# Kernel optimization log

Measured on AMD Instinct MI355X. Metric: run time of the kernel, lower is better.

Reference implementation:

```python
import jax, jax.numpy as jnp
import numpy as np

MODEL_DIMS = 1024
NUM_LAYERS = 4
NUM_SUPPORT = 256


def setup_inputs() -> dict:
    key = jax.random.key(0)
    kx, kk, kv = jax.random.split(key, 3)
    x = jax.random.normal(kx, (4, 4096, MODEL_DIMS), dtype=jnp.float32)
    # Stacked per-layer parameters, matching nn.Parameter(torch.randn(...))
    keys = jax.random.normal(kk, (NUM_LAYERS, NUM_SUPPORT, MODEL_DIMS), dtype=jnp.float32)
    values = jax.random.normal(kv, (NUM_LAYERS, NUM_SUPPORT, MODEL_DIMS), dtype=jnp.float32)
    return {"x": x, "keys": keys, "values": values}


def reference(x, keys, values):
    # Chain of CleanUpKV layers: normalize -> scores -> softmax -> weighted values.
    def step(h, kv):
        k, v = kv  # k, v: [num_support, D]
        hn = h / (jnp.linalg.norm(h, axis=-1, keepdims=True) + 1e-9)
        scores = jnp.einsum('bsd,nd->bsn', hn, k)          # [B,S,num_support]
        w = jax.nn.softmax(scores, axis=-1)
        return jnp.einsum('bsn,nd->bsd', w, v), None

    out, _ = jax.lax.scan(step, x, (keys, values))
    return out
```

## Files before the change

### kernel.cpp

```cpp
#include <hip/hip_runtime.h>
#include <hip/hip_bf16.h>
#include <stdint.h>

#define D 1024
#define NSUP 256
#define ROWS 16384
#define MB 64
#define LTHREADS 512

typedef __attribute__((__ext_vector_type__(8))) __bf16 bf16x8;
typedef __attribute__((__ext_vector_type__(4))) float f32x4;

__device__ __forceinline__ float bfbits2f(uint32_t b) {
    union { uint32_t u; float f; } c; c.u = b; return c.f;
}

__device__ __forceinline__ int hnb(int row, int d) {
    return ((row << 8) + (d << 1)) ^ ((row & 7) << 4);
}
__device__ __forceinline__ int wbyte(int row, int n) {
    return ((row << 9) + (n << 1)) ^ ((row & 7) << 4);
}

__global__ void cast_k_kernel(const float* __restrict__ K, __bf16* __restrict__ Kb) {
    int i = (blockIdx.x * 256 + threadIdx.x) * 4;
    float4 v = *(const float4*)(K + i);
    __bf16 o[4] __attribute__((aligned(8)));
    o[0] = (__bf16)v.x; o[1] = (__bf16)v.y; o[2] = (__bf16)v.z; o[3] = (__bf16)v.w;
    *(uint2*)(Kb + i) = *(const uint2*)o;
}

__global__ void transpose_v_kernel(const float* __restrict__ V, __bf16* __restrict__ Vt) {
    __shared__ __bf16 tile[64][72];
    int l = blockIdx.z;
    int d0 = blockIdx.x * 64, n0 = blockIdx.y * 64;
    const float* Vl = V + (size_t)l * NSUP * D;
    __bf16* Vtl = Vt + (size_t)l * D * NSUP;
    for (int j = 0; j < 16; ++j) {
        int idx = j * 256 + threadIdx.x;
        int n_l = idx >> 6, d_l = idx & 63;
        tile[d_l][n_l] = (__bf16)Vl[(size_t)(n0 + n_l) * D + d0 + d_l];
    }
    __syncthreads();
    for (int j = 0; j < 16; ++j) {
        int idx = j * 256 + threadIdx.x;
        int d_l = idx >> 6, n_l = idx & 63;
        Vtl[(size_t)(d0 + d_l) * NSUP + n0 + n_l] = tile[d_l][n_l];
    }
}

__global__ void norms0_kernel(const float* __restrict__ x, float* __restrict__ rn) {
    int row = blockIdx.x * 4 + (threadIdx.x >> 6);
    int lane = threadIdx.x & 63;
    const float4* p = (const float4*)(x + (size_t)row * D);
    float s = 0.f;
    #pragma unroll
    for (int j = 0; j < 4; ++j) {
        float4 v = p[j * 64 + lane];
        s += v.x * v.x + v.y * v.y + v.z * v.z + v.w * v.w;
    }
    #pragma unroll
    for (int off = 1; off < 64; off <<= 1) s += __shfl_xor(s, off);
    if (lane == 0) rn[row] = 1.f / (sqrtf(s) + 1e-9f);
}

template<bool IN_F32, bool OUT_F32>
__global__ __launch_bounds__(LTHREADS)
void layer_kernel(const void* h_in, void* h_out,
                  const __bf16* __restrict__ Kb, const __bf16* __restrict__ Vt,
                  const float* __restrict__ rn_in, float* __restrict__ rn_out) {
    const int tid = threadIdx.x;
    const int lane = tid & 63;
    const int cg = tid >> 6;
    const int llo = lane & 15, lhi = lane >> 4;
    const int row0 = blockIdx.x * MB;

    __shared__ __align__(16) char lds_hn[2][MB * 128 * 2];
    __shared__ __align__(16) char lds_w[MB * NSUP * 2];
    __shared__ float red1[MB][8];
    __shared__ float red2[MB][8];
    __shared__ float rnin_s[MB];

    if (tid < MB) rnin_s[tid] = rn_in[row0 + tid];

    const int srow = tid >> 3;
    const int sd = (tid & 7) * 16;

    float stg[16];
    auto load_chunk = [&](int dc) {
        if constexpr (IN_F32) {
            const float4* p = (const float4*)((const float*)h_in + (size_t)(row0 + srow) * D + dc * 128 + sd);
            #pragma unroll
            for (int j = 0; j < 4; ++j) {
                float4 v = p[j];
                stg[4 * j] = v.x; stg[4 * j + 1] = v.y; stg[4 * j + 2] = v.z; stg[4 * j + 3] = v.w;
            }
        } else {
            const uint4* p = (const uint4*)((const uint16_t*)h_in + (size_t)(row0 + srow) * D + dc * 128 + sd);
            #pragma unroll
            for (int j = 0; j < 2; ++j) {
                uint4 u = p[j];
                uint32_t wv[4] = {u.x, u.y, u.z, u.w};
                #pragma unroll
                for (int q = 0; q < 4; ++q) {
                    stg[8 * j + 2 * q]     = bfbits2f(wv[q] << 16);
                    stg[8 * j + 2 * q + 1] = bfbits2f(wv[q] & 0xffff0000u);
                }
            }
        }
    };
    auto write_chunk = [&](int dc) {
        float rn = rnin_s[srow];
        __bf16 tmp[16] __attribute__((aligned(16)));
        #pragma unroll
        for (int j = 0; j < 16; ++j) tmp[j] = (__bf16)(stg[j] * rn);
        char* base = lds_hn[dc & 1];
        *(bf16x8*)(base + hnb(srow, sd))     = *(const bf16x8*)(tmp);
        *(bf16x8*)(base + hnb(srow, sd + 8)) = *(const bf16x8*)(tmp + 8);
    };

    f32x4 acc[4][2];
    #pragma unroll
    for (int rf = 0; rf < 4; ++rf)
        #pragma unroll
        for (int cf = 0; cf < 2; ++cf)
            acc[rf][cf] = (f32x4){0.f, 0.f, 0.f, 0.f};

    load_chunk(0);
    #pragma unroll 1
    for (int dc = 0; dc < 8; ++dc) {
        __syncthreads();
        write_chunk(dc);
        if (dc < 7) load_chunk(dc + 1);
        __syncthreads();
        const char* hb = lds_hn[dc & 1];
        #pragma unroll
        for (int k = 0; k < 4; ++k) {
            bf16x8 a[4];
            #pragma unroll
            for (int rf = 0; rf < 4; ++rf)
                a[rf] = *(const bf16x8*)(hb + hnb(rf * 16 + llo, k * 32 + lhi * 8));
            #pragma unroll
            for (int cf = 0; cf < 2; ++cf) {
                const __bf16* kp = Kb + (size_t)(cg * 32 + cf * 16 + llo) * D + dc * 128 + k * 32 + lhi * 8;
                bf16x8 b = *(const bf16x8*)kp;
                #pragma unroll
                for (int rf = 0; rf < 4; ++rf)
                    acc[rf][cf] = __builtin_amdgcn_mfma_f32_16x16x32_bf16(a[rf], b, acc[rf][cf], 0, 0, 0);
            }
        }
    }

    float rmax[4][4];
    #pragma unroll
    for (int rf = 0; rf < 4; ++rf)
        #pragma unroll
        for (int r = 0; r < 4; ++r) {
            float m = fmaxf(acc[rf][0][r], acc[rf][1][r]);
            #pragma unroll
            for (int off = 1; off < 16; off <<= 1) m = fmaxf(m, __shfl_xor(m, off));
            rmax[rf][r] = m;
        }
    if (llo == 0) {
        #pragma unroll
        for (int rf = 0; rf < 4; ++rf)
            #pragma unroll
            for (int r = 0; r < 4; ++r)
                red1[rf * 16 + lhi * 4 + r][cg] = rmax[rf][r];
    }
    __syncthreads();
    #pragma unroll
    for (int rf = 0; rf < 4; ++rf)
        #pragma unroll
        for (int r = 0; r < 4; ++r) {
            int row = rf * 16 + lhi * 4 + r;
            f32x4 m0 = *(const f32x4*)&red1[row][0];
            f32x4 m1 = *(const f32x4*)&red1[row][4];
            float m = fmaxf(fmaxf(fmaxf(m0[0], m0[1]), fmaxf(m0[2], m0[3])),
                            fmaxf(fmaxf(m1[0], m1[1]), fmaxf(m1[2], m1[3])));
            rmax[rf][r] = m;
        }
    float rsum[4][4];
    #pragma unroll
    for (int rf = 0; rf < 4; ++rf)
        #pragma unroll
        for (int r = 0; r < 4; ++r) {
            float s = 0.f;
            #pragma unroll
            for (int cf = 0; cf < 2; ++cf) {
                float e = exp2f((acc[rf][cf][r] - rmax[rf][r]) * 1.44269504f);
                acc[rf][cf][r] = e;
                s += e;
            }
            #pragma unroll
            for (int off = 1; off < 16; off <<= 1) s += __shfl_xor(s, off);
            rsum[rf][r] = s;
        }
    if (llo == 0) {
        #pragma unroll
        for (int rf = 0; rf < 4; ++rf)
            #pragma unroll
            for (int r = 0; r < 4; ++r)
                red2[rf * 16 + lhi * 4 + r][cg] = rsum[rf][r];
    }
    __syncthreads();
    #pragma unroll
    for (int rf = 0; rf < 4; ++rf)
        #pragma unroll
        for (int r = 0; r < 4; ++r) {
            int row = rf * 16 + lhi * 4 + r;
            f32x4 s0 = *(const f32x4*)&red2[row][0];
            f32x4 s1 = *(const f32x4*)&red2[row][4];
            float s = (s0[0] + s0[1] + s0[2] + s0[3]) + (s1[0] + s1[1] + s1[2] + s1[3]);
            float inv = 1.f / s;
            #pragma unroll
            for (int cf = 0; cf < 2; ++cf) {
                int col = cg * 32 + cf * 16 + llo;
                *(__bf16*)(lds_w + wbyte(row, col)) = (__bf16)(acc[rf][cf][r] * inv);
            }
        }
    __syncthreads();

    float nacc[4][4];
    #pragma unroll
    for (int rf = 0; rf < 4; ++rf)
        #pragma unroll
        for (int r = 0; r < 4; ++r) nacc[rf][r] = 0.f;

    #pragma unroll 1
    for (int dchunk = 0; dchunk < 2; ++dchunk) {
        f32x4 acc2[4][4];
        #pragma unroll
        for (int rf = 0; rf < 4; ++rf)
            #pragma unroll
            for (int cf = 0; cf < 4; ++cf)
                acc2[rf][cf] = (f32x4){0.f, 0.f, 0.f, 0.f};
        #pragma unroll
        for (int k = 0; k < 8; ++k) {
            bf16x8 a[4];
            #pragma unroll
            for (int rf = 0; rf < 4; ++rf)
                a[rf] = *(const bf16x8*)(lds_w + wbyte(rf * 16 + llo, k * 32 + lhi * 8));
            #pragma unroll
            for (int cf = 0; cf < 4; ++cf) {
                const __bf16* vp = Vt + (size_t)(cg * 128 + dchunk * 64 + cf * 16 + llo) * NSUP + k * 32 + lhi * 8;
                bf16x8 b = *(const bf16x8*)vp;
                #pragma unroll
                for (int rf = 0; rf < 4; ++rf)
                    acc2[rf][cf] = __builtin_amdgcn_mfma_f32_16x16x32_bf16(a[rf], b, acc2[rf][cf], 0, 0, 0);
            }
        }
        #pragma unroll
        for (int rf = 0; rf < 4; ++rf)
            #pragma unroll
            for (int cf = 0; cf < 4; ++cf) {
                int d = cg * 128 + dchunk * 64 + cf * 16 + llo;
                #pragma unroll
                for (int r = 0; r < 4; ++r) {
                    int row = rf * 16 + lhi * 4 + r;
                    float v = acc2[rf][cf][r];
                    size_t idx = (size_t)(row0 + row) * D + d;
                    if constexpr (OUT_F32) {
                        ((float*)h_out)[idx] = v;
                    } else {
                        ((__bf16*)h_out)[idx] = (__bf16)v;
                        nacc[rf][r] += v * v;
                    }
                }
            }
    }

    if constexpr (!OUT_F32) {
        #pragma unroll
        for (int rf = 0; rf < 4; ++rf)
            #pragma unroll
            for (int r = 0; r < 4; ++r) {
                float s = nacc[rf][r];
                #pragma unroll
                for (int off = 1; off < 16; off <<= 1) s += __shfl_xor(s, off);
                nacc[rf][r] = s;
            }
        if (llo == 0) {
            #pragma unroll
            for (int rf = 0; rf < 4; ++rf)
                #pragma unroll
                for (int r = 0; r < 4; ++r)
                    red1[rf * 16 + lhi * 4 + r][cg] = nacc[rf][r];
        }
        __syncthreads();
        if (cg == 0 && llo == 0) {
            #pragma unroll
            for (int rf = 0; rf < 4; ++rf)
                #pragma unroll
                for (int r = 0; r < 4; ++r) {
                    int row = rf * 16 + lhi * 4 + r;
                    f32x4 s0 = *(const f32x4*)&red1[row][0];
                    f32x4 s1 = *(const f32x4*)&red1[row][4];
                    float ss = (s0[0] + s0[1] + s0[2] + s0[3]) + (s1[0] + s1[1] + s1[2] + s1[3]);
                    rn_out[row0 + row] = 1.f / (sqrtf(ss) + 1e-9f);
                }
        }
    }
}

extern "C" void kernel_launch(void* const* d_in, const int* in_sizes, int n_in,
                              void* d_out, int out_size, void* d_ws, size_t ws_size,
                              hipStream_t stream) {
    const float* x = (const float*)d_in[0];
    const float* keys = (const float*)d_in[1];
    const float* values = (const float*)d_in[2];
    float* out = (float*)d_out;

    char* ws = (char*)d_ws;
    __bf16* h   = (__bf16*)(ws);
    __bf16* Kb  = (__bf16*)(ws + 33554432);
    __bf16* Vt  = (__bf16*)(ws + 35651584);
    float*  rn0 = (float*)(ws + 37748736);
    float*  rn1 = (float*)(ws + 37814272);

    cast_k_kernel<<<1024, 256, 0, stream>>>(keys, Kb);
    transpose_v_kernel<<<dim3(16, 4, 4), 256, 0, stream>>>(values, Vt);
    norms0_kernel<<<4096, 256, 0, stream>>>(x, rn0);

    const int LSTRIDE = NSUP * D;
    layer_kernel<true,  false><<<256, LTHREADS, 0, stream>>>(x, h, Kb,               Vt,               rn0, rn1);
    layer_kernel<false, false><<<256, LTHREADS, 0, stream>>>(h, h, Kb + LSTRIDE,     Vt + LSTRIDE,     rn1, rn0);
    layer_kernel<false, false><<<256, LTHREADS, 0, stream>>>(h, h, Kb + 2 * LSTRIDE, Vt + 2 * LSTRIDE, rn0, rn1);
    layer_kernel<false, true ><<<256, LTHREADS, 0, stream>>>(h, out, Kb + 3 * LSTRIDE, Vt + 3 * LSTRIDE, rn1, nullptr);
}
```

Before: 268.5 us.

## Halve row tile, store pre-normalized bf16 activations, use direct global-to-LDS loads

Shrinks the row block from 64 to 32, which doubles the grid to 512 blocks. Occupancy is raised with launch bounds of 4 blocks per SM. The separate norms kernel is folded into the first layer. Later layers now store normalized bf16 activations, so the next layer can stream them straight into LDS with global_load_lds and skip the per-element conversion. Output writes for intermediate layers are staged through swizzled LDS so they become coalesced 16-byte stores. In exchange, each block gets fewer MFMAs per K/V load, and global K/V traffic per row doubles.

```diff
diff --git a/kernel.cpp b/kernel.cpp
--- a/kernel.cpp
+++ b/kernel.cpp
@@ -5,22 +5,17 @@
 #define D 1024
 #define NSUP 256
 #define ROWS 16384
-#define MB 64
+#define MB 32
 #define LTHREADS 512
+#define LGRID (ROWS / MB)
 
 typedef __attribute__((__ext_vector_type__(8))) __bf16 bf16x8;
 typedef __attribute__((__ext_vector_type__(4))) float f32x4;
-
-__device__ __forceinline__ float bfbits2f(uint32_t b) {
-    union { uint32_t u; float f; } c; c.u = b; return c.f;
-}
-
-__device__ __forceinline__ int hnb(int row, int d) {
-    return ((row << 8) + (d << 1)) ^ ((row & 7) << 4);
-}
-__device__ __forceinline__ int wbyte(int row, int n) {
-    return ((row << 9) + (n << 1)) ^ ((row & 7) << 4);
-}
+typedef __attribute__((__ext_vector_type__(4))) uint32_t u32x4;
+
+#define MFMA16(a, b, c) __builtin_amdgcn_mfma_f32_16x16x32_bf16((a), (b), (c), 0, 0, 0)
+
+__device__ __forceinline__ int swz(int row, int byte) { return byte ^ ((row & 7) << 4); }
 
 __global__ void cast_k_kernel(const float* __restrict__ K, __bf16* __restrict__ Kb) {
     int i = (blockIdx.x * 256 + threadIdx.x) * 4;
@@ -49,128 +44,119 @@
     }
 }
 
-__global__ void norms0_kernel(const float* __restrict__ x, float* __restrict__ rn) {
-    int row = blockIdx.x * 4 + (threadIdx.x >> 6);
-    int lane = threadIdx.x & 63;
-    const float4* p = (const float4*)(x + (size_t)row * D);
-    float s = 0.f;
-    #pragma unroll
-    for (int j = 0; j < 4; ++j) {
-        float4 v = p[j * 64 + lane];
-        s += v.x * v.x + v.y * v.y + v.z * v.z + v.w * v.w;
-    }
-    #pragma unroll
-    for (int off = 1; off < 64; off <<= 1) s += __shfl_xor(s, off);
-    if (lane == 0) rn[row] = 1.f / (sqrtf(s) + 1e-9f);
-}
-
 template<bool IN_F32, bool OUT_F32>
-__global__ __launch_bounds__(LTHREADS)
-void layer_kernel(const void* h_in, void* h_out,
-                  const __bf16* __restrict__ Kb, const __bf16* __restrict__ Vt,
-                  const float* __restrict__ rn_in, float* __restrict__ rn_out) {
+__global__ __launch_bounds__(LTHREADS, 4)
+void layer_kernel(const void* __restrict__ h_in, void* __restrict__ h_out,
+                  const __bf16* __restrict__ Kb, const __bf16* __restrict__ Vt) {
     const int tid = threadIdx.x;
     const int lane = tid & 63;
     const int cg = tid >> 6;
     const int llo = lane & 15, lhi = lane >> 4;
     const int row0 = blockIdx.x * MB;
 
-    __shared__ __align__(16) char lds_hn[2][MB * 128 * 2];
-    __shared__ __align__(16) char lds_w[MB * NSUP * 2];
+    __shared__ __align__(16) char pool[49152];
     __shared__ float red1[MB][8];
     __shared__ float red2[MB][8];
     __shared__ float rnin_s[MB];
 
-    if (tid < MB) rnin_s[tid] = rn_in[row0 + tid];
-
-    const int srow = tid >> 3;
-    const int sd = (tid & 7) * 16;
-
-    float stg[16];
-    auto load_chunk = [&](int dc) {
+    char* wbuf = pool + 32768;
+
+    if constexpr (IN_F32) {
+        const float4* x4 = (const float4*)h_in;
+        #pragma unroll
+        for (int rr = 0; rr < 4; ++rr) {
+            int row = cg * 4 + rr;
+            const float4* p = x4 + (size_t)(row0 + row) * 256;
+            float s = 0.f;
+            #pragma unroll
+            for (int j = 0; j < 4; ++j) {
+                float4 v = p[j * 64 + lane];
+                s += v.x * v.x + v.y * v.y + v.z * v.z + v.w * v.w;
+            }
+            #pragma unroll
+            for (int off = 1; off < 64; off <<= 1) s += __shfl_xor(s, off);
+            if (lane == 0) rnin_s[row] = 1.f / (sqrtf(s) + 1e-9f);
+        }
+        __syncthreads();
+    }
+
+    auto stage = [&](int dc) {
+        char* hb = pool + (dc & 1) * 16384;
         if constexpr (IN_F32) {
-            const float4* p = (const float4*)((const float*)h_in + (size_t)(row0 + srow) * D + dc * 128 + sd);
-            #pragma unroll
-            for (int j = 0; j < 4; ++j) {
-                float4 v = p[j];
-                stg[4 * j] = v.x; stg[4 * j + 1] = v.y; stg[4 * j + 2] = v.z; stg[4 * j + 3] = v.w;
-            }
+            int srow = tid >> 4;
+            int sd = (tid & 15) * 16;
+            const float4* p = (const float4*)((const float*)h_in + (size_t)(row0 + srow) * D + dc * 256 + sd);
+            float rn = rnin_s[srow];
+            __bf16 tmp[16] __attribute__((aligned(16)));
+            #pragma unroll
+            for (int q = 0; q < 4; ++q) {
+                float4 v = p[q];
+                tmp[4 * q + 0] = (__bf16)(v.x * rn);
+                tmp[4 * q + 1] = (__bf16)(v.y * rn);
+                tmp[4 * q + 2] = (__bf16)(v.z * rn);
+                tmp[4 * q + 3] = (__bf16)(v.w * rn);
+            }
+            char* base = hb + srow * 512;
+            *(bf16x8*)(base + swz(srow, sd * 2))      = *(const bf16x8*)(tmp);
+            *(bf16x8*)(base + swz(srow, sd * 2 + 16)) = *(const bf16x8*)(tmp + 8);
         } else {
-            const uint4* p = (const uint4*)((const uint16_t*)h_in + (size_t)(row0 + srow) * D + dc * 128 + sd);
-            #pragma unroll
-            for (int j = 0; j < 2; ++j) {
-                uint4 u = p[j];
-                uint32_t wv[4] = {u.x, u.y, u.z, u.w};
-                #pragma unroll
-                for (int q = 0; q < 4; ++q) {
-                    stg[8 * j + 2 * q]     = bfbits2f(wv[q] << 16);
-                    stg[8 * j + 2 * q + 1] = bfbits2f(wv[q] & 0xffff0000u);
-                }
+            #pragma unroll
+            for (int c = 0; c < 2; ++c) {
+                int row = c * 16 + (tid >> 5);
+                int seg = tid & 31;
+                const char* g = (const char*)h_in + (size_t)(row0 + row) * 2048 + (size_t)dc * 512
+                                + swz(row, seg * 16);
+                char* l = hb + row * 512 + seg * 16;
+                __builtin_amdgcn_global_load_lds(
+                    (const __attribute__((address_space(1))) uint32_t*)g,
+                    (__attribute__((address_space(3))) uint32_t*)l, 16, 0, 0);
             }
         }
     };
-    auto write_chunk = [&](int dc) {
-        float rn = rnin_s[srow];
-        __bf16 tmp[16] __attribute__((aligned(16)));
-        #pragma unroll
-        for (int j = 0; j < 16; ++j) tmp[j] = (__bf16)(stg[j] * rn);
-        char* base = lds_hn[dc & 1];
-        *(bf16x8*)(base + hnb(srow, sd))     = *(const bf16x8*)(tmp);
-        *(bf16x8*)(base + hnb(srow, sd + 8)) = *(const bf16x8*)(tmp + 8);
-    };
-
-    f32x4 acc[4][2];
-    #pragma unroll
-    for (int rf = 0; rf < 4; ++rf)
+
+    f32x4 acc[2][2];
+    #pragma unroll
+    for (int rf = 0; rf < 2; ++rf)
         #pragma unroll
         for (int cf = 0; cf < 2; ++cf)
             acc[rf][cf] = (f32x4){0.f, 0.f, 0.f, 0.f};
 
-    load_chunk(0);
+    stage(0);
+    __syncthreads();
     #pragma unroll 1
-    for (int dc = 0; dc < 8; ++dc) {
+    for (int dc = 0; dc < 4; ++dc) {
+        if (dc < 3) stage(dc + 1);
+        const char* hb = pool + (dc & 1) * 16384;
+        #pragma unroll
+        for (int k = 0; k < 8; ++k) {
+            bf16x8 a0 = *(const bf16x8*)(hb + llo * 512 + swz(llo, k * 64 + lhi * 16));
+            bf16x8 a1 = *(const bf16x8*)(hb + (16 + llo) * 512 + swz(16 + llo, k * 64 + lhi * 16));
+            #pragma unroll
+            for (int cf = 0; cf < 2; ++cf) {
+                bf16x8 b = *(const bf16x8*)(Kb + (size_t)(cg * 32 + cf * 16 + llo) * D
+                                            + dc * 256 + k * 32 + lhi * 8);
+                acc[0][cf] = MFMA16(a0, b, acc[0][cf]);
+                acc[1][cf] = MFMA16(a1, b, acc[1][cf]);
+            }
+        }
         __syncthreads();
-        write_chunk(dc);
-        if (dc < 7) load_chunk(dc + 1);
-        __syncthreads();
-        const char* hb = lds_hn[dc & 1];
-        #pragma unroll
-        for (int k = 0; k < 4; ++k) {
-            bf16x8 a[4];
-            #pragma unroll
-            for (int rf = 0; rf < 4; ++rf)
-                a[rf] = *(const bf16x8*)(hb + hnb(rf * 16 + llo, k * 32 + lhi * 8));
-            #pragma unroll
-            for (int cf = 0; cf < 2; ++cf) {
-                const __bf16* kp = Kb + (size_t)(cg * 32 + cf * 16 + llo) * D + dc * 128 + k * 32 + lhi * 8;
-                bf16x8 b = *(const bf16x8*)kp;
-                #pragma unroll
-                for (int rf = 0; rf < 4; ++rf)
-                    acc[rf][cf] = __builtin_amdgcn_mfma_f32_16x16x32_bf16(a[rf], b, acc[rf][cf], 0, 0, 0);
-            }
-        }
-    }
-
-    float rmax[4][4];
-    #pragma unroll
-    for (int rf = 0; rf < 4; ++rf)
+    }
+
+    float rmax[2][4];
+    #pragma unroll
+    for (int rf = 0; rf < 2; ++rf)
         #pragma unroll
         for (int r = 0; r < 4; ++r) {
             float m = fmaxf(acc[rf][0][r], acc[rf][1][r]);
             #pragma unroll
             for (int off = 1; off < 16; off <<= 1) m = fmaxf(m, __shfl_xor(m, off));
             rmax[rf][r] = m;
-        }
-    if (llo == 0) {
-        #pragma unroll
-        for (int rf = 0; rf < 4; ++rf)
-            #pragma unroll
-            for (int r = 0; r < 4; ++r)
-                red1[rf * 16 + lhi * 4 + r][cg] = rmax[rf][r];
-    }
-    __syncthreads();
-    #pragma unroll
-    for (int rf = 0; rf < 4; ++rf)
+            if (llo == 0) red1[rf * 16 + lhi * 4 + r][cg] = m;
+        }
+    __syncthreads();
+    float rsum[2][4];
+    #pragma unroll
+    for (int rf = 0; rf < 2; ++rf)
         #pragma unroll
         for (int r = 0; r < 4; ++r) {
             int row = rf * 16 + lhi * 4 + r;
@@ -178,34 +164,21 @@
             f32x4 m1 = *(const f32x4*)&red1[row][4];
             float m = fmaxf(fmaxf(fmaxf(m0[0], m0[1]), fmaxf(m0[2], m0[3])),
                             fmaxf(fmaxf(m1[0], m1[1]), fmaxf(m1[2], m1[3])));
-            rmax[rf][r] = m;
-        }
-    float rsum[4][4];
-    #pragma unroll
-    for (int rf = 0; rf < 4; ++rf)
-        #pragma unroll
-        for (int r = 0; r < 4; ++r) {
             float s = 0.f;
             #pragma unroll
             for (int cf = 0; cf < 2; ++cf) {
-                float e = exp2f((acc[rf][cf][r] - rmax[rf][r]) * 1.44269504f);
+                float e = exp2f((acc[rf][cf][r] - m) * 1.44269504f);
                 acc[rf][cf][r] = e;
                 s += e;
             }
             #pragma unroll
             for (int off = 1; off < 16; off <<= 1) s += __shfl_xor(s, off);
             rsum[rf][r] = s;
-        }
-    if (llo == 0) {
-        #pragma unroll
-        for (int rf = 0; rf < 4; ++rf)
-            #pragma unroll
-            for (int r = 0; r < 4; ++r)
-                red2[rf * 16 + lhi * 4 + r][cg] = rsum[rf][r];
-    }
-    __syncthreads();
-    #pragma unroll
-    for (int rf = 0; rf < 4; ++rf)
+            if (llo == 0) red2[row][cg] = s;
+        }
+    __syncthreads();
+    #pragma unroll
+    for (int rf = 0; rf < 2; ++rf)
         #pragma unroll
         for (int r = 0; r < 4; ++r) {
             int row = rf * 16 + lhi * 4 + r;
@@ -216,89 +189,97 @@
             #pragma unroll
             for (int cf = 0; cf < 2; ++cf) {
                 int col = cg * 32 + cf * 16 + llo;
-                *(__bf16*)(lds_w + wbyte(row, col)) = (__bf16)(acc[rf][cf][r] * inv);
-            }
-        }
-    __syncthreads();
-
-    float nacc[4][4];
-    #pragma unroll
-    for (int rf = 0; rf < 4; ++rf)
-        #pragma unroll
-        for (int r = 0; r < 4; ++r) nacc[rf][r] = 0.f;
-
-    #pragma unroll 1
-    for (int dchunk = 0; dchunk < 2; ++dchunk) {
-        f32x4 acc2[4][4];
-        #pragma unroll
-        for (int rf = 0; rf < 4; ++rf)
-            #pragma unroll
-            for (int cf = 0; cf < 4; ++cf)
-                acc2[rf][cf] = (f32x4){0.f, 0.f, 0.f, 0.f};
-        #pragma unroll
-        for (int k = 0; k < 8; ++k) {
-            bf16x8 a[4];
-            #pragma unroll
-            for (int rf = 0; rf < 4; ++rf)
-                a[rf] = *(const bf16x8*)(lds_w + wbyte(rf * 16 + llo, k * 32 + lhi * 8));
-            #pragma unroll
-            for (int cf = 0; cf < 4; ++cf) {
-                const __bf16* vp = Vt + (size_t)(cg * 128 + dchunk * 64 + cf * 16 + llo) * NSUP + k * 32 + lhi * 8;
-                bf16x8 b = *(const bf16x8*)vp;
-                #pragma unroll
-                for (int rf = 0; rf < 4; ++rf)
-                    acc2[rf][cf] = __builtin_amdgcn_mfma_f32_16x16x32_bf16(a[rf], b, acc2[rf][cf], 0, 0, 0);
-            }
-        }
-        #pragma unroll
-        for (int rf = 0; rf < 4; ++rf)
-            #pragma unroll
-            for (int cf = 0; cf < 4; ++cf) {
-                int d = cg * 128 + dchunk * 64 + cf * 16 + llo;
+                *(__bf16*)(wbuf + row * 512 + swz(row, col * 2)) = (__bf16)(acc[rf][cf][r] * inv);
+            }
+        }
+    __syncthreads();
+
+    f32x4 acc2[2][8];
+    #pragma unroll
+    for (int rf = 0; rf < 2; ++rf)
+        #pragma unroll
+        for (int cf = 0; cf < 8; ++cf)
+            acc2[rf][cf] = (f32x4){0.f, 0.f, 0.f, 0.f};
+
+    #pragma unroll
+    for (int k = 0; k < 8; ++k) {
+        bf16x8 a0 = *(const bf16x8*)(wbuf + llo * 512 + swz(llo, k * 64 + lhi * 16));
+        bf16x8 a1 = *(const bf16x8*)(wbuf + (16 + llo) * 512 + swz(16 + llo, k * 64 + lhi * 16));
+        #pragma unroll
+        for (int cf = 0; cf < 8; ++cf) {
+            bf16x8 b = *(const bf16x8*)(Vt + (size_t)(cg * 128 + cf * 16 + llo) * NSUP
+                                        + k * 32 + lhi * 8);
+            acc2[0][cf] = MFMA16(a0, b, acc2[0][cf]);
+            acc2[1][cf] = MFMA16(a1, b, acc2[1][cf]);
+        }
+    }
+
+    if constexpr (OUT_F32) {
+        float* outp = (float*)h_out;
+        #pragma unroll
+        for (int rf = 0; rf < 2; ++rf)
+            #pragma unroll
+            for (int cf = 0; cf < 8; ++cf) {
+                int d = cg * 128 + cf * 16 + llo;
                 #pragma unroll
                 for (int r = 0; r < 4; ++r) {
                     int row = rf * 16 + lhi * 4 + r;
-                    float v = acc2[rf][cf][r];
-                    size_t idx = (size_t)(row0 + row) * D + d;
-                    if constexpr (OUT_F32) {
-                        ((float*)h_out)[idx] = v;
-                    } else {
-                        ((__bf16*)h_out)[idx] = (__bf16)v;
-                        nacc[rf][r] += v * v;
+                    outp[(size_t)(row0 + row) * D + d] = acc2[rf][cf][r];
+                }
+            }
+    } else {
+        float rnv[2][4];
+        #pragma unroll
+        for (int rf = 0; rf < 2; ++rf)
+            #pragma unroll
+            for (int r = 0; r < 4; ++r) {
+                float s = 0.f;
+                #pragma unroll
+                for (int cf = 0; cf < 8; ++cf) s += acc2[rf][cf][r] * acc2[rf][cf][r];
+                #pragma unroll
+                for (int off = 1; off < 16; off <<= 1) s += __shfl_xor(s, off);
+                if (llo == 0) red2[rf * 16 + lhi * 4 + r][cg] = s;
+            }
+        __syncthreads();
+        #pragma unroll
+        for (int rf = 0; rf < 2; ++rf)
+            #pragma unroll
+            for (int r = 0; r < 4; ++r) {
+                int row = rf * 16 + lhi * 4 + r;
+                f32x4 s0 = *(const f32x4*)&red2[row][0];
+                f32x4 s1 = *(const f32x4*)&red2[row][4];
+                float ss = (s0[0] + s0[1] + s0[2] + s0[3]) + (s1[0] + s1[1] + s1[2] + s1[3]);
+                rnv[rf][r] = 1.f / (sqrtf(ss) + 1e-9f);
+            }
+        const int myhalf = cg >> 2;
+        char* epi = pool;
+        #pragma unroll 1
+        for (int hh = 0; hh < 2; ++hh) {
+            if (myhalf == hh) {
+                #pragma unroll
+                for (int rf = 0; rf < 2; ++rf)
+                    #pragma unroll
+                    for (int cf = 0; cf < 8; ++cf) {
+                        int dcol = (cg & 3) * 128 + cf * 16 + llo;
+                        #pragma unroll
+                        for (int r = 0; r < 4; ++r) {
+                            int row = rf * 16 + lhi * 4 + r;
+                            *(__bf16*)(epi + row * 1024 + swz(row, dcol * 2)) =
+                                (__bf16)(acc2[rf][cf][r] * rnv[rf][r]);
+                        }
                     }
+            }
+            __syncthreads();
+            {
+                int row = tid >> 4;
+                #pragma unroll
+                for (int j = 0; j < 4; ++j) {
+                    int seg = (tid & 15) + 16 * j;
+                    u32x4 v = *(const u32x4*)(epi + row * 1024 + swz(row, seg * 16));
+                    *(u32x4*)((char*)h_out + (size_t)(row0 + row) * 2048 + hh * 1024 + seg * 16) = v;
                 }
             }
-    }
-
-    if constexpr (!OUT_F32) {
-        #pragma unroll
-        for (int rf = 0; rf < 4; ++rf)
-            #pragma unroll
-            for (int r = 0; r < 4; ++r) {
-                float s = nacc[rf][r];
-                #pragma unroll
-                for (int off = 1; off < 16; off <<= 1) s += __shfl_xor(s, off);
-                nacc[rf][r] = s;
-            }
-        if (llo == 0) {
-            #pragma unroll
-            for (int rf = 0; rf < 4; ++rf)
-                #pragma unroll
-                for (int r = 0; r < 4; ++r)
-                    red1[rf * 16 + lhi * 4 + r][cg] = nacc[rf][r];
-        }
-        __syncthreads();
-        if (cg == 0 && llo == 0) {
-            #pragma unroll
-            for (int rf = 0; rf < 4; ++rf)
-                #pragma unroll
-                for (int r = 0; r < 4; ++r) {
-                    int row = rf * 16 + lhi * 4 + r;
-                    f32x4 s0 = *(const f32x4*)&red1[row][0];
-                    f32x4 s1 = *(const f32x4*)&red1[row][4];
-                    float ss = (s0[0] + s0[1] + s0[2] + s0[3]) + (s1[0] + s1[1] + s1[2] + s1[3]);
-                    rn_out[row0 + row] = 1.f / (sqrtf(ss) + 1e-9f);
-                }
+            __syncthreads();
         }
     }
 }
@@ -312,19 +293,16 @@
     float* out = (float*)d_out;
 
     char* ws = (char*)d_ws;
-    __bf16* h   = (__bf16*)(ws);
-    __bf16* Kb  = (__bf16*)(ws + 33554432);
-    __bf16* Vt  = (__bf16*)(ws + 35651584);
-    float*  rn0 = (float*)(ws + 37748736);
-    float*  rn1 = (float*)(ws + 37814272);
+    __bf16* h  = (__bf16*)(ws);
+    __bf16* Kb = (__bf16*)(ws + 33554432);
+    __bf16* Vt = (__bf16*)(ws + 35651584);
 
     cast_k_kernel<<<1024, 256, 0, stream>>>(keys, Kb);
     transpose_v_kernel<<<dim3(16, 4, 4), 256, 0, stream>>>(values, Vt);
-    norms0_kernel<<<4096, 256, 0, stream>>>(x, rn0);
-
-    const int LSTRIDE = NSUP * D;
-    layer_kernel<true,  false><<<256, LTHREADS, 0, stream>>>(x, h, Kb,               Vt,               rn0, rn1);
-    layer_kernel<false, false><<<256, LTHREADS, 0, stream>>>(h, h, Kb + LSTRIDE,     Vt + LSTRIDE,     rn1, rn0);
-    layer_kernel<false, false><<<256, LTHREADS, 0, stream>>>(h, h, Kb + 2 * LSTRIDE, Vt + 2 * LSTRIDE, rn0, rn1);
-    layer_kernel<false, true ><<<256, LTHREADS, 0, stream>>>(h, out, Kb + 3 * LSTRIDE, Vt + 3 * LSTRIDE, rn1, nullptr);
+
+    const int LS = NSUP * D;
+    layer_kernel<true,  false><<<LGRID, LTHREADS, 0, stream>>>(x, h, Kb,          Vt);
+    layer_kernel<false, false><<<LGRID, LTHREADS, 0, stream>>>(h, h, Kb + LS,     Vt + LS);
+    layer_kernel<false, false><<<LGRID, LTHREADS, 0, stream>>>(h, h, Kb + 2 * LS, Vt + 2 * LS);
+    layer_kernel<false, true ><<<LGRID, LTHREADS, 0, stream>>>(h, out, Kb + 3 * LS, Vt + 3 * LS);
 }
```

Result: slower. 344.4 us (+28.2%).
